# Kernel optimization log

Measured on AMD Instinct MI355X. Metric: run time of the kernel, lower is better.

The kernel has to match this reference:

```python
import jax, jax.numpy as jnp
import numpy as np

THRESHOLD = 0.5


def _crop_resize(img, hstart, ch, wstart, cw, out_h, out_w):
    # Bilinear resample (TF half-pixel-centers) of the crop
    # img[hstart:hstart+ch, wstart:wstart+cw] up to (out_h, out_w).
    chf = ch.astype(jnp.float32)
    cwf = cw.astype(jnp.float32)
    ys = jnp.clip((jnp.arange(out_h, dtype=jnp.float32) + 0.5) * (chf / out_h) - 0.5,
                  0.0, chf - 1.0) + hstart
    xs = jnp.clip((jnp.arange(out_w, dtype=jnp.float32) + 0.5) * (cwf / out_w) - 0.5,
                  0.0, cwf - 1.0) + wstart
    y0 = jnp.floor(ys).astype(jnp.int32)
    y1 = jnp.minimum(y0 + 1, hstart + ch - 1)
    x0 = jnp.floor(xs).astype(jnp.int32)
    x1 = jnp.minimum(x0 + 1, wstart + cw - 1)
    wy = (ys - y0)[:, None, None]
    wx = (xs - x0)[None, :, None]
    r0 = img[y0]  # (out_h, W, C) gathered rows
    r1 = img[y1]
    top = (1.0 - wx) * r0[:, x0] + wx * r0[:, x1]
    bot = (1.0 - wx) * r1[:, x0] + wx * r1[:, x1]
    return (1.0 - wy) * top + wy * bot


def _per_sample(mask, img):
    H, W = img.shape[0], img.shape[1]
    m = (mask >= THRESHOLD).astype(img.dtype)  # (H, W, 1)
    masked = m * img                           # (H, W, C)
    rows = jnp.sum(m[..., 0], axis=1)          # row sums (H,)
    cols = jnp.sum(m[..., 0], axis=0)          # col sums (W,)
    # bbox: first nonzero index - 1 (clamped to 0), last nonzero index + 1
    xl = jnp.maximum(jnp.argmax(rows > 0).astype(jnp.int32) - 1, 0)
    xr = (H - jnp.argmax((rows > 0)[::-1])).astype(jnp.int32)
    yl = jnp.maximum(jnp.argmax(cols > 0).astype(jnp.int32) - 1, 0)
    yr = (W - jnp.argmax((cols > 0)[::-1])).astype(jnp.int32)
    h = xr - xl
    w = yr - yl
    # smart_resize with square target: center-crop bbox to square side min(h, w)
    c = jnp.minimum(h, w)
    hstart = xl + (h - c) // 2
    wstart = yl + (w - c) // 2
    return _crop_resize(masked, hstart, c, wstart, c, H, W)


def setup_inputs() -> dict:
    key = jax.random.key(0)
    k1, k2 = jax.random.split(key)
    masks = jax.random.uniform(k1, (16, 1024, 1024, 1), dtype=jnp.float32)
    images = jax.random.uniform(k2, (16, 1024, 1024, 3), dtype=jnp.float32)
    return {"masks": masks, "images": images}


def reference(masks, images):
    return jax.vmap(_per_sample)(masks, images)
```

## Files before the change

kernel.cpp:

```cpp
#include <hip/hip_runtime.h>

#define HH 1024
#define WW 1024
#define NS 16

__global__ __launch_bounds__(256)
void pack_kernel(const float* __restrict__ mask,
                 unsigned int* __restrict__ packed,
                 int* __restrict__ rowMinC,
                 int* __restrict__ rowMaxC) {
    const int row = blockIdx.x;
    const int s   = blockIdx.y;
    const int t   = threadIdx.x;

    const float4* m4 = (const float4*)(mask + ((size_t)s * HH + row) * WW);
    float4 v = m4[t];
    unsigned int n = (v.x >= 0.5f ? 1u : 0u)
                   | (v.y >= 0.5f ? 2u : 0u)
                   | (v.z >= 0.5f ? 4u : 0u)
                   | (v.w >= 0.5f ? 8u : 0u);

    __shared__ unsigned char nib[256];
    nib[t] = (unsigned char)n;

    int col = t << 2;
    int cmin = WW, cmax = -1;
    if (n) {
        cmin = (n & 1) ? col : ((n & 2) ? col + 1 : ((n & 4) ? col + 2 : col + 3));
        cmax = (n & 8) ? col + 3 : ((n & 4) ? col + 2 : ((n & 2) ? col + 1 : col));
    }
    for (int off = 32; off > 0; off >>= 1) {
        cmin = min(cmin, __shfl_down(cmin, off));
        cmax = max(cmax, __shfl_down(cmax, off));
    }
    __shared__ int sm[4][2];
    int wave = t >> 6, lane = t & 63;
    if (lane == 0) { sm[wave][0] = cmin; sm[wave][1] = cmax; }
    __syncthreads();

    if (t < 32) {
        unsigned int w = 0;
        const unsigned char* p = &nib[t << 3];
#pragma unroll
        for (int j = 0; j < 8; ++j) w |= ((unsigned int)p[j]) << (j << 2);
        packed[((size_t)s * HH + row) * 32 + t] = w;
    }
    if (t == 0) {
        for (int wv = 1; wv < 4; ++wv) {
            cmin = min(cmin, sm[wv][0]);
            cmax = max(cmax, sm[wv][1]);
        }
        rowMinC[s * HH + row] = cmin;
        rowMaxC[s * HH + row] = cmax;
    }
}

__global__ __launch_bounds__(256)
void reduce_kernel(const int* __restrict__ rowMinC,
                   const int* __restrict__ rowMaxC,
                   int* __restrict__ bbox) {
    const int s = blockIdx.x;
    const int t = threadIdx.x;
    int minR = HH, maxR = -1, minC = WW, maxC = -1;
    for (int m = 0; m < HH / 256; ++m) {
        int r = t + (m << 8);
        int mc = rowMaxC[s * HH + r];
        if (mc >= 0) {
            minR = min(minR, r);
            maxR = max(maxR, r);
            minC = min(minC, rowMinC[s * HH + r]);
            maxC = max(maxC, mc);
        }
    }
    for (int off = 32; off > 0; off >>= 1) {
        minR = min(minR, __shfl_down(minR, off));
        maxR = max(maxR, __shfl_down(maxR, off));
        minC = min(minC, __shfl_down(minC, off));
        maxC = max(maxC, __shfl_down(maxC, off));
    }
    __shared__ int sm[4][4];
    int wave = t >> 6, lane = t & 63;
    if (lane == 0) { sm[wave][0] = minR; sm[wave][1] = maxR; sm[wave][2] = minC; sm[wave][3] = maxC; }
    __syncthreads();
    if (t == 0) {
        for (int wv = 1; wv < 4; ++wv) {
            minR = min(minR, sm[wv][0]);
            maxR = max(maxR, sm[wv][1]);
            minC = min(minC, sm[wv][2]);
            maxC = max(maxC, sm[wv][3]);
        }
        bbox[s * 4 + 0] = minR;
        bbox[s * 4 + 1] = maxR;
        bbox[s * 4 + 2] = minC;
        bbox[s * 4 + 3] = maxC;
    }
}

__global__ __launch_bounds__(256)
void resize_kernel(const float* __restrict__ mask,
                   const float* __restrict__ img,
                   const unsigned int* __restrict__ packed,
                   const int* __restrict__ bbox,
                   float* __restrict__ out) {
    const int row = blockIdx.x;
    const int s   = blockIdx.y;
    const int t   = threadIdx.x;

    __shared__ unsigned int pw[32];
    if (t < 32) pw[t] = packed[((size_t)s * HH + row) * 32 + t];

    int minR = bbox[s * 4 + 0], maxR = bbox[s * 4 + 1];
    int minC = bbox[s * 4 + 2], maxC = bbox[s * 4 + 3];
    int xl, xr, yl, yr;
    if (maxR < 0) { xl = 0; xr = HH; } else { xl = max(minR - 1, 0); xr = maxR + 1; }
    if (maxC < 0) { yl = 0; yr = WW; } else { yl = max(minC - 1, 0); yr = maxC + 1; }
    int h = xr - xl, w = yr - yl;
    int c = min(h, w);
    int hstart = xl + (h - c) / 2;
    int wstart = yl + (w - c) / 2;

    const float* im   = img + (size_t)s * HH * WW * 3;
    float*       orow = out + ((size_t)s * HH + row) * WW * 3;

    __syncthreads();

    if (c == HH && c == WW && hstart == 0 && wstart == 0) {
        const float4* ip = (const float4*)(im + (size_t)row * WW * 3);
        float4*       op = (float4*)orow;
#pragma unroll
        for (int j = 0; j < 3; ++j) {
            int fi = t + (j << 8);
            int F  = fi << 2;
            int p0 = F / 3;
            int r  = F - p0 * 3;
            unsigned int b0 = (pw[p0 >> 5] >> (p0 & 31)) & 1u;
            int p1 = p0 + 1;
            unsigned int b1 = (pw[p1 >> 5] >> (p1 & 31)) & 1u;
            float4 v = ip[fi];
            float4 o;
            o.x = b0 ? v.x : 0.0f;
            o.y = ((r < 2) ? b0 : b1) ? v.y : 0.0f;
            o.z = ((r == 0) ? b0 : b1) ? v.z : 0.0f;
            o.w = b1 ? v.w : 0.0f;
            op[fi] = o;
        }
        return;
    }

    const float* msk = mask + (size_t)s * HH * WW;
    float cf = (float)c;
    float sy = cf / (float)HH;
    float sx = cf / (float)WW;

    float ysf = fminf(fmaxf((row + 0.5f) * sy - 0.5f, 0.0f), cf - 1.0f);
    int   y0i = (int)floorf(ysf);
    float wy  = ysf - (float)y0i;
    int   ry0 = hstart + y0i;
    int   ry1 = min(ry0 + 1, hstart + c - 1);

    for (int k = 0; k < 4; ++k) {
        int ox = (t << 2) + k;
        float xsf = fminf(fmaxf((ox + 0.5f) * sx - 0.5f, 0.0f), cf - 1.0f);
        int   x0i = (int)floorf(xsf);
        float wx  = xsf - (float)x0i;
        int   rx0 = wstart + x0i;
        int   rx1 = min(rx0 + 1, wstart + c - 1);

        float p00[3], p01[3], p10[3], p11[3];
        auto fetch = [&](int y, int x, float* p) {
            int idx = y * WW + x;
            float mv = msk[idx];
            if (mv >= 0.5f) {
                const float* q = im + (size_t)idx * 3;
                p[0] = q[0]; p[1] = q[1]; p[2] = q[2];
            } else {
                p[0] = 0.0f; p[1] = 0.0f; p[2] = 0.0f;
            }
        };
        fetch(ry0, rx0, p00);
        fetch(ry0, rx1, p01);
        fetch(ry1, rx0, p10);
        fetch(ry1, rx1, p11);

        float* o = orow + (size_t)ox * 3;
#pragma unroll
        for (int ch = 0; ch < 3; ++ch) {
            float top = (1.0f - wx) * p00[ch] + wx * p01[ch];
            float bot = (1.0f - wx) * p10[ch] + wx * p11[ch];
            o[ch] = (1.0f - wy) * top + wy * bot;
        }
    }
}

extern "C" void kernel_launch(void* const* d_in, const int* in_sizes, int n_in,
                              void* d_out, int out_size, void* d_ws, size_t ws_size,
                              hipStream_t stream) {
    const float* masks  = (const float*)d_in[0];
    const float* images = (const float*)d_in[1];
    float* out = (float*)d_out;

    int* ws            = (int*)d_ws;
    int* bbox          = ws;
    int* rowMinC       = ws + 64;
    int* rowMaxC       = rowMinC + NS * HH;
    unsigned int* pk   = (unsigned int*)(rowMaxC + NS * HH);

    pack_kernel  <<<dim3(HH, NS), 256, 0, stream>>>(masks, pk, rowMinC, rowMaxC);
    reduce_kernel<<<NS,           256, 0, stream>>>(rowMinC, rowMaxC, bbox);
    resize_kernel<<<dim3(HH, NS), 256, 0, stream>>>(masks, images, pk, bbox, out);
}
```

Before: 94.03 us.

## Fuse bbox reduction into resize kernel and process eight rows per block

Removes the separate reduce kernel. Every resize block now recomputes the per-sample bbox from rowMinC/rowMaxC, which cuts out one launch and its serialization gap. Both the pack and resize kernels now handle 8 rows per block, which reduces block count and scheduling overhead. Packing switches from shared-memory nibbles to warp shuffles with ctz/clz. The cost is a redundant 1024-row reduction in each of the 128 blocks per sample, and fewer blocks in flight for latency hiding.

```diff
diff --git a/kernel.cpp b/kernel.cpp
--- a/kernel.cpp
+++ b/kernel.cpp
@@ -3,66 +3,74 @@
 #define HH 1024
 #define WW 1024
 #define NS 16
+#define ROWS_PER_BLOCK 8
+#define BLOCKS_X (HH / ROWS_PER_BLOCK)
 
 __global__ __launch_bounds__(256)
 void pack_kernel(const float* __restrict__ mask,
                  unsigned int* __restrict__ packed,
                  int* __restrict__ rowMinC,
                  int* __restrict__ rowMaxC) {
-    const int row = blockIdx.x;
-    const int s   = blockIdx.y;
-    const int t   = threadIdx.x;
-
-    const float4* m4 = (const float4*)(mask + ((size_t)s * HH + row) * WW);
-    float4 v = m4[t];
-    unsigned int n = (v.x >= 0.5f ? 1u : 0u)
-                   | (v.y >= 0.5f ? 2u : 0u)
-                   | (v.z >= 0.5f ? 4u : 0u)
-                   | (v.w >= 0.5f ? 8u : 0u);
-
-    __shared__ unsigned char nib[256];
-    nib[t] = (unsigned char)n;
-
-    int col = t << 2;
-    int cmin = WW, cmax = -1;
-    if (n) {
-        cmin = (n & 1) ? col : ((n & 2) ? col + 1 : ((n & 4) ? col + 2 : col + 3));
-        cmax = (n & 8) ? col + 3 : ((n & 4) ? col + 2 : ((n & 2) ? col + 1 : col));
-    }
-    for (int off = 32; off > 0; off >>= 1) {
-        cmin = min(cmin, __shfl_down(cmin, off));
-        cmax = max(cmax, __shfl_down(cmax, off));
-    }
-    __shared__ int sm[4][2];
-    int wave = t >> 6, lane = t & 63;
-    if (lane == 0) { sm[wave][0] = cmin; sm[wave][1] = cmax; }
+    const int s  = blockIdx.y;
+    const int r0 = blockIdx.x * ROWS_PER_BLOCK;
+    const int t  = threadIdx.x;
+
+    const float4* m4 = (const float4*)(mask + (size_t)s * HH * WW);
+    __shared__ int smin[ROWS_PER_BLOCK][4], smax[ROWS_PER_BLOCK][4];
+
+#pragma unroll
+    for (int rr = 0; rr < ROWS_PER_BLOCK; ++rr) {
+        const int row = r0 + rr;
+        float4 v = m4[(size_t)row * 256 + t];
+        unsigned int w = (v.x >= 0.5f ? 1u : 0u)
+                       | (v.y >= 0.5f ? 2u : 0u)
+                       | (v.z >= 0.5f ? 4u : 0u)
+                       | (v.w >= 0.5f ? 8u : 0u);
+        w |= __shfl_down(w, 1) << 4;
+        w |= __shfl_down(w, 2) << 8;
+        w |= __shfl_down(w, 4) << 16;
+
+        int cmin = WW, cmax = -1;
+        if ((t & 7) == 0) {
+            int g = t >> 3;
+            packed[((size_t)s * HH + row) * 32 + g] = w;
+            if (w) {
+                cmin = (g << 5) + __builtin_ctz(w);
+                cmax = (g << 5) + 31 - __builtin_clz(w);
+            }
+        }
+        for (int off = 32; off > 0; off >>= 1) {
+            cmin = min(cmin, __shfl_down(cmin, off));
+            cmax = max(cmax, __shfl_down(cmax, off));
+        }
+        if ((t & 63) == 0) { smin[rr][t >> 6] = cmin; smax[rr][t >> 6] = cmax; }
+    }
     __syncthreads();
-
-    if (t < 32) {
-        unsigned int w = 0;
-        const unsigned char* p = &nib[t << 3];
-#pragma unroll
-        for (int j = 0; j < 8; ++j) w |= ((unsigned int)p[j]) << (j << 2);
-        packed[((size_t)s * HH + row) * 32 + t] = w;
-    }
-    if (t == 0) {
-        for (int wv = 1; wv < 4; ++wv) {
-            cmin = min(cmin, sm[wv][0]);
-            cmax = max(cmax, sm[wv][1]);
-        }
-        rowMinC[s * HH + row] = cmin;
-        rowMaxC[s * HH + row] = cmax;
+    if (t < ROWS_PER_BLOCK) {
+        int cmin = min(min(smin[t][0], smin[t][1]), min(smin[t][2], smin[t][3]));
+        int cmax = max(max(smax[t][0], smax[t][1]), max(smax[t][2], smax[t][3]));
+        rowMinC[s * HH + r0 + t] = cmin;
+        rowMaxC[s * HH + r0 + t] = cmax;
     }
 }
 
 __global__ __launch_bounds__(256)
-void reduce_kernel(const int* __restrict__ rowMinC,
+void resize_kernel(const float* __restrict__ mask,
+                   const float* __restrict__ img,
+                   const unsigned int* __restrict__ packed,
+                   const int* __restrict__ rowMinC,
                    const int* __restrict__ rowMaxC,
-                   int* __restrict__ bbox) {
-    const int s = blockIdx.x;
-    const int t = threadIdx.x;
+                   float* __restrict__ out) {
+    const int s  = blockIdx.y;
+    const int r0 = blockIdx.x * ROWS_PER_BLOCK;
+    const int t  = threadIdx.x;
+
+    __shared__ unsigned int pw[ROWS_PER_BLOCK][32];
+    pw[t >> 5][t & 31] = packed[((size_t)s * HH + r0) * 32 + t];
+
     int minR = HH, maxR = -1, minC = WW, maxC = -1;
-    for (int m = 0; m < HH / 256; ++m) {
+#pragma unroll
+    for (int m = 0; m < 4; ++m) {
         int r = t + (m << 8);
         int mc = rowMaxC[s * HH + r];
         if (mc >= 0) {
@@ -79,6 +87,7 @@
         maxC = max(maxC, __shfl_down(maxC, off));
     }
     __shared__ int sm[4][4];
+    __shared__ int bc[3];
     int wave = t >> 6, lane = t & 63;
     if (lane == 0) { sm[wave][0] = minR; sm[wave][1] = maxR; sm[wave][2] = minC; sm[wave][3] = maxC; }
     __syncthreads();
@@ -89,60 +98,45 @@
             minC = min(minC, sm[wv][2]);
             maxC = max(maxC, sm[wv][3]);
         }
-        bbox[s * 4 + 0] = minR;
-        bbox[s * 4 + 1] = maxR;
-        bbox[s * 4 + 2] = minC;
-        bbox[s * 4 + 3] = maxC;
-    }
-}
-
-__global__ __launch_bounds__(256)
-void resize_kernel(const float* __restrict__ mask,
-                   const float* __restrict__ img,
-                   const unsigned int* __restrict__ packed,
-                   const int* __restrict__ bbox,
-                   float* __restrict__ out) {
-    const int row = blockIdx.x;
-    const int s   = blockIdx.y;
-    const int t   = threadIdx.x;
-
-    __shared__ unsigned int pw[32];
-    if (t < 32) pw[t] = packed[((size_t)s * HH + row) * 32 + t];
-
-    int minR = bbox[s * 4 + 0], maxR = bbox[s * 4 + 1];
-    int minC = bbox[s * 4 + 2], maxC = bbox[s * 4 + 3];
-    int xl, xr, yl, yr;
-    if (maxR < 0) { xl = 0; xr = HH; } else { xl = max(minR - 1, 0); xr = maxR + 1; }
-    if (maxC < 0) { yl = 0; yr = WW; } else { yl = max(minC - 1, 0); yr = maxC + 1; }
-    int h = xr - xl, w = yr - yl;
-    int c = min(h, w);
-    int hstart = xl + (h - c) / 2;
-    int wstart = yl + (w - c) / 2;
-
-    const float* im   = img + (size_t)s * HH * WW * 3;
-    float*       orow = out + ((size_t)s * HH + row) * WW * 3;
-
+        int xl, xr, yl, yr;
+        if (maxR < 0) { xl = 0; xr = HH; } else { xl = max(minR - 1, 0); xr = maxR + 1; }
+        if (maxC < 0) { yl = 0; yr = WW; } else { yl = max(minC - 1, 0); yr = maxC + 1; }
+        int h = xr - xl, w = yr - yl;
+        int c = min(h, w);
+        bc[0] = c;
+        bc[1] = xl + (h - c) / 2;
+        bc[2] = yl + (w - c) / 2;
+    }
     __syncthreads();
+    const int c = bc[0], hstart = bc[1], wstart = bc[2];
+
+    const float* im = img + (size_t)s * HH * WW * 3;
+    float*      ob  = out + (size_t)s * HH * WW * 3;
 
     if (c == HH && c == WW && hstart == 0 && wstart == 0) {
-        const float4* ip = (const float4*)(im + (size_t)row * WW * 3);
-        float4*       op = (float4*)orow;
-#pragma unroll
-        for (int j = 0; j < 3; ++j) {
-            int fi = t + (j << 8);
-            int F  = fi << 2;
-            int p0 = F / 3;
-            int r  = F - p0 * 3;
-            unsigned int b0 = (pw[p0 >> 5] >> (p0 & 31)) & 1u;
-            int p1 = p0 + 1;
-            unsigned int b1 = (pw[p1 >> 5] >> (p1 & 31)) & 1u;
-            float4 v = ip[fi];
-            float4 o;
-            o.x = b0 ? v.x : 0.0f;
-            o.y = ((r < 2) ? b0 : b1) ? v.y : 0.0f;
-            o.z = ((r == 0) ? b0 : b1) ? v.z : 0.0f;
-            o.w = b1 ? v.w : 0.0f;
-            op[fi] = o;
+        const float4* ip = (const float4*)(im + (size_t)r0 * WW * 3);
+        float4*       op = (float4*)(ob + (size_t)r0 * WW * 3);
+#pragma unroll
+        for (int rr = 0; rr < ROWS_PER_BLOCK; ++rr) {
+            const unsigned int* pwr = pw[rr];
+#pragma unroll
+            for (int j = 0; j < 3; ++j) {
+                int fi = t + (j << 8);
+                int F  = fi << 2;
+                int p0 = F / 3;
+                int r  = F - p0 * 3;
+                unsigned int b0 = (pwr[p0 >> 5] >> (p0 & 31)) & 1u;
+                int p1 = p0 + 1;
+                unsigned int b1 = (pwr[p1 >> 5] >> (p1 & 31)) & 1u;
+                size_t off = (size_t)rr * 768 + fi;
+                float4 v = ip[off];
+                float4 o;
+                o.x = b0 ? v.x : 0.0f;
+                o.y = ((r < 2) ? b0 : b1) ? v.y : 0.0f;
+                o.z = ((r == 0) ? b0 : b1) ? v.z : 0.0f;
+                o.w = b1 ? v.w : 0.0f;
+                op[off] = o;
+            }
         }
         return;
     }
@@ -152,42 +146,46 @@
     float sy = cf / (float)HH;
     float sx = cf / (float)WW;
 
-    float ysf = fminf(fmaxf((row + 0.5f) * sy - 0.5f, 0.0f), cf - 1.0f);
-    int   y0i = (int)floorf(ysf);
-    float wy  = ysf - (float)y0i;
-    int   ry0 = hstart + y0i;
-    int   ry1 = min(ry0 + 1, hstart + c - 1);
-
-    for (int k = 0; k < 4; ++k) {
-        int ox = (t << 2) + k;
-        float xsf = fminf(fmaxf((ox + 0.5f) * sx - 0.5f, 0.0f), cf - 1.0f);
-        int   x0i = (int)floorf(xsf);
-        float wx  = xsf - (float)x0i;
-        int   rx0 = wstart + x0i;
-        int   rx1 = min(rx0 + 1, wstart + c - 1);
-
-        float p00[3], p01[3], p10[3], p11[3];
-        auto fetch = [&](int y, int x, float* p) {
-            int idx = y * WW + x;
-            float mv = msk[idx];
-            if (mv >= 0.5f) {
-                const float* q = im + (size_t)idx * 3;
-                p[0] = q[0]; p[1] = q[1]; p[2] = q[2];
-            } else {
-                p[0] = 0.0f; p[1] = 0.0f; p[2] = 0.0f;
+    for (int rr = 0; rr < ROWS_PER_BLOCK; ++rr) {
+        const int row = r0 + rr;
+        float ysf = fminf(fmaxf((row + 0.5f) * sy - 0.5f, 0.0f), cf - 1.0f);
+        int   y0i = (int)floorf(ysf);
+        float wy  = ysf - (float)y0i;
+        int   ry0 = hstart + y0i;
+        int   ry1 = min(ry0 + 1, hstart + c - 1);
+        float* orow = ob + (size_t)row * WW * 3;
+
+        for (int k = 0; k < 4; ++k) {
+            int ox = (t << 2) + k;
+            float xsf = fminf(fmaxf((ox + 0.5f) * sx - 0.5f, 0.0f), cf - 1.0f);
+            int   x0i = (int)floorf(xsf);
+            float wx  = xsf - (float)x0i;
+            int   rx0 = wstart + x0i;
+            int   rx1 = min(rx0 + 1, wstart + c - 1);
+
+            float p00[3], p01[3], p10[3], p11[3];
+            auto fetch = [&](int y, int x, float* p) {
+                int idx = y * WW + x;
+                float mv = msk[idx];
+                if (mv >= 0.5f) {
+                    const float* q = im + (size_t)idx * 3;
+                    p[0] = q[0]; p[1] = q[1]; p[2] = q[2];
+                } else {
+                    p[0] = 0.0f; p[1] = 0.0f; p[2] = 0.0f;
+                }
+            };
+            fetch(ry0, rx0, p00);
+            fetch(ry0, rx1, p01);
+            fetch(ry1, rx0, p10);
+            fetch(ry1, rx1, p11);
+
+            float* o = orow + (size_t)ox * 3;
+#pragma unroll
+            for (int ch = 0; ch < 3; ++ch) {
+                float top = (1.0f - wx) * p00[ch] + wx * p01[ch];
+                float bot = (1.0f - wx) * p10[ch] + wx * p11[ch];
+                o[ch] = (1.0f - wy) * top + wy * bot;
             }
-        };
-        fetch(ry0, rx0, p00);
-        fetch(ry0, rx1, p01);
-        fetch(ry1, rx0, p10);
-        fetch(ry1, rx1, p11);
-
-        float* o = orow + (size_t)ox * 3;
-#pragma unroll
-        for (int ch = 0; ch < 3; ++ch) {
-            float top = (1.0f - wx) * p00[ch] + wx * p01[ch];
-            float bot = (1.0f - wx) * p10[ch] + wx * p11[ch];
-            o[ch] = (1.0f - wy) * top + wy * bot;
         }
     }
 }
@@ -199,13 +197,10 @@
     const float* images = (const float*)d_in[1];
     float* out = (float*)d_out;
 
-    int* ws            = (int*)d_ws;
-    int* bbox          = ws;
-    int* rowMinC       = ws + 64;
-    int* rowMaxC       = rowMinC + NS * HH;
-    unsigned int* pk   = (unsigned int*)(rowMaxC + NS * HH);
-
-    pack_kernel  <<<dim3(HH, NS), 256, 0, stream>>>(masks, pk, rowMinC, rowMaxC);
-    reduce_kernel<<<NS,           256, 0, stream>>>(rowMinC, rowMaxC, bbox);
-    resize_kernel<<<dim3(HH, NS), 256, 0, stream>>>(masks, images, pk, bbox, out);
+    int* rowMinC     = (int*)d_ws;
+    int* rowMaxC     = rowMinC + NS * HH;
+    unsigned int* pk = (unsigned int*)(rowMaxC + NS * HH);
+
+    pack_kernel  <<<dim3(BLOCKS_X, NS), 256, 0, stream>>>(masks, pk, rowMinC, rowMaxC);
+    resize_kernel<<<dim3(BLOCKS_X, NS), 256, 0, stream>>>(masks, images, pk, rowMinC, rowMaxC, out);
 }
```

Measured after the change: 100.3 us. 1.07x slower.
